# Kernel tuning notes

Hardware: AMD Instinct MI355X
Metric: run time of the kernel (lower is better)

The kernel has to match this reference:

```python
import jax, jax.numpy as jnp
import numpy as np

HEADS = 4
DIM_HEAD = 32
DIM = 128
HIDDEN = HEADS * DIM_HEAD  # 128
LN_EPS = 1e-6


def setup_inputs() -> dict:
    key = jax.random.key(0)
    ks = jax.random.split(key, 4)
    b, X, Y, Z = 4, 32, 32, 32
    x = jax.random.normal(ks[0], (b, X, Y, Z, DIM), dtype=jnp.float32)
    # 1x1x1 convs are pointwise linears: kernel [in, out]
    w_qkv = jax.random.normal(ks[1], (DIM, 3 * HIDDEN), dtype=jnp.float32) * (DIM ** -0.5)
    w_out = jax.random.normal(ks[2], (HIDDEN, DIM), dtype=jnp.float32) * (HIDDEN ** -0.5)
    b_out = jax.random.normal(ks[3], (DIM,), dtype=jnp.float32) * 0.02
    ln_scale = jnp.ones((DIM,), dtype=jnp.float32)
    ln_bias = jnp.zeros((DIM,), dtype=jnp.float32)
    return {"x": x, "w_qkv": w_qkv, "w_out": w_out, "b_out": b_out,
            "ln_scale": ln_scale, "ln_bias": ln_bias}


def reference(x, w_qkv, w_out, b_out, ln_scale, ln_bias):
    b, X, Y, Z, c = x.shape
    n = X * Y * Z
    scale = DIM_HEAD ** (-0.5)

    # 1x1x1 conv (no bias) == pointwise matmul over channels
    qkv = jnp.einsum('bxyzc,cd->bxyzd', x, w_qkv)  # [b,X,Y,Z,3*hidden]
    q, k, v = jnp.split(qkv, 3, axis=-1)

    # rearrange 'b x y z (h c) -> b h c n'
    def to_bhcn(t):
        return t.reshape(b, n, HEADS, DIM_HEAD).transpose(0, 2, 3, 1)

    q, k, v = to_bhcn(q), to_bhcn(k), to_bhcn(v)

    q = jax.nn.softmax(q, axis=-2) * scale   # softmax over feature dim d
    k = jax.nn.softmax(k, axis=-1)           # softmax over token dim n

    context = jnp.einsum('bhdn,bhcn->bhdc', k, v)   # [b,h,d,c] small d=c=32
    out = jnp.einsum('bhde,bhdn->bhen', context, q) # [b,h,e,n]

    # rearrange 'b h c n -> b x y z (h c)' (cubic volume, matching original)
    out = out.transpose(0, 3, 1, 2).reshape(b, X, Y, Z, HIDDEN)

    # final 1x1x1 conv with bias
    out = jnp.einsum('bxyzh,hc->bxyzc', out, w_out) + b_out

    # LayerNorm over last axis (flax default eps=1e-6, with scale+bias)
    mu = jnp.mean(out, axis=-1, keepdims=True)
    var = jnp.mean(jnp.square(out - mu), axis=-1, keepdims=True)
    out = (out - mu) * jax.lax.rsqrt(var + LN_EPS) * ln_scale + ln_bias
    return out
```

## Files before the change

kernel.cpp:

```cpp
#include <hip/hip_runtime.h>
#include <hip/hip_bf16.h>

typedef _Float16 f16;
typedef _Float16 f16x4 __attribute__((ext_vector_type(4)));
typedef _Float16 f16x8 __attribute__((ext_vector_type(8)));
typedef float f32x4 __attribute__((ext_vector_type(4)));

#define MFMA(a, b, c) __builtin_amdgcn_mfma_f32_16x16x32_f16((a), (b), (c), 0, 0, 0)

#define BB 4
#define NPOS 32768
#define HH 4
#define NBLK 1024
#define NBLK3 4096
#define STATB 2304
#define LDP 136

__device__ __forceinline__ f16x8 ldx8(const float* p) {
  float4 a = *(const float4*)p;
  float4 b = *(const float4*)(p + 4);
  return (f16x8){(f16)a.x, (f16)a.y, (f16)a.z, (f16)a.w,
                 (f16)b.x, (f16)b.y, (f16)b.z, (f16)b.w};
}

__global__ __launch_bounds__(256)
void la_k0_prep(const float* __restrict__ wqkv, f16* __restrict__ wkvF,
                f16* __restrict__ wqF) {
  const int g0 = blockIdx.x * 256 + threadIdx.x;
  for (int i = g0; i < 32768; i += 16384) {
    int j = i & 7, l = (i >> 3) & 63, ks = (i >> 9) & 3, nt = (i >> 11) & 3,
        h = i >> 13;
    int n = 16 * nt + (l & 15);
    int c = 32 * ks + 8 * (l >> 4) + j;
    int col = (n < 32) ? (128 + h * 32 + n) : (256 + h * 32 + (n - 32));
    wkvF[i] = (f16)wqkv[c * 384 + col];
  }
  {
    int i = g0;
    int j = i & 7, l = (i >> 3) & 63, ks = (i >> 9) & 3, a = (i >> 11) & 1,
        h = i >> 12;
    int row = l & 15;
    int n = 8 * (row >> 2) + 4 * a + (row & 3);
    int c = 32 * ks + 8 * (l >> 4) + j;
    wqF[i] = (f16)wqkv[c * 384 + h * 32 + n];
  }
}

__global__ __launch_bounds__(256, 4)
void la_k1_stats(const float* __restrict__ x, const f16* __restrict__ wkvF,
                 const f16* __restrict__ wqF, char* __restrict__ stats,
                 f16* __restrict__ Qhat) {
  const int blk = blockIdx.x, t = threadIdx.x;
  const int w = t >> 6, l = t & 63, lg = l >> 4, ln = l & 15;

  __shared__ __align__(16) f16 EV[64 * LDP];

  const float* xb = x + (size_t)blk * (128 * 128);
  f16x8 xf[2][4];
#pragma unroll
  for (int mi = 0; mi < 2; ++mi)
#pragma unroll
    for (int ks = 0; ks < 4; ++ks)
      xf[mi][ks] = ldx8(xb + (32 * w + 16 * mi + ln) * 128 + 32 * ks + 8 * lg);

  const f32x4 Z4 = {0.f, 0.f, 0.f, 0.f};

#pragma unroll 1
  for (int h = 0; h < HH; ++h) {
    f32x4 acc[2][4];
#pragma unroll
    for (int mi = 0; mi < 2; ++mi)
#pragma unroll
      for (int nt = 0; nt < 4; ++nt) acc[mi][nt] = Z4;
#pragma unroll
    for (int ks = 0; ks < 4; ++ks) {
#pragma unroll
      for (int nt = 0; nt < 4; ++nt) {
        f16x8 bf = *(const f16x8*)(wkvF + (((h * 4 + nt) * 4 + ks) << 9) + l * 8);
        acc[0][nt] = MFMA(xf[0][ks], bf, acc[0][nt]);
        acc[1][nt] = MFMA(xf[1][ks], bf, acc[1][nt]);
      }
    }

    {
      float sl[2] = {0.f, 0.f};
#pragma unroll
      for (int nt = 0; nt < 2; ++nt)
#pragma unroll
        for (int mi = 0; mi < 2; ++mi) {
          float e0 = __expf(acc[mi][nt][0]);
          float e1 = __expf(acc[mi][nt][1]);
          float e2 = __expf(acc[mi][nt][2]);
          float e3 = __expf(acc[mi][nt][3]);
          sl[nt] += (e0 + e1) + (e2 + e3);
          *(f16x4*)&EV[(16 * nt + ln) * LDP + 32 * w + 16 * mi + 4 * lg] =
              (f16x4){(f16)e0, (f16)e1, (f16)e2, (f16)e3};
          f32x4 vv = acc[mi][nt + 2];
          *(f16x4*)&EV[(32 + 16 * nt + ln) * LDP + 32 * w + 16 * mi + 4 * lg] =
              (f16x4){(f16)vv[0], (f16)vv[1], (f16)vv[2], (f16)vv[3]};
        }
#pragma unroll
      for (int nt = 0; nt < 2; ++nt) {
        sl[nt] += __shfl_xor(sl[nt], 16);
        sl[nt] += __shfl_xor(sl[nt], 32);
      }
      f16* sp = (f16*)(stats + (size_t)(blk * HH + h) * STATB + 2048);
      if (lg == 0) {
        sp[ln * 4 + w] = (f16)sl[0];
        sp[(16 + ln) * 4 + w] = (f16)sl[1];
      }
    }

    __syncthreads();

    {
      const int tm = w >> 1, tn = w & 1;
      f32x4 tacc = Z4;
#pragma unroll
      for (int ks = 0; ks < 4; ++ks) {
        f16x8 ea = *(const f16x8*)&EV[(16 * tm + ln) * LDP + 32 * ks + 8 * lg];
        f16x8 vb = *(const f16x8*)&EV[(32 + 16 * tn + ln) * LDP + 32 * ks + 8 * lg];
        tacc = MFMA(ea, vb, tacc);
      }
      f16* tp = (f16*)(stats + (size_t)(blk * HH + h) * STATB);
#pragma unroll
      for (int r = 0; r < 4; ++r)
        tp[(16 * tm + 4 * lg + r) * 32 + 16 * tn + ln] = (f16)tacc[r];
    }

    {
      f32x4 qa[2][2];
#pragma unroll
      for (int mi = 0; mi < 2; ++mi)
#pragma unroll
        for (int a = 0; a < 2; ++a) qa[mi][a] = Z4;
#pragma unroll
      for (int ks = 0; ks < 4; ++ks) {
        f16x8 a0 = *(const f16x8*)(wqF + (((h * 2 + 0) * 4 + ks) << 9) + l * 8);
        f16x8 a1 = *(const f16x8*)(wqF + (((h * 2 + 1) * 4 + ks) << 9) + l * 8);
#pragma unroll
        for (int mi = 0; mi < 2; ++mi) {
          qa[mi][0] = MFMA(a0, xf[mi][ks], qa[mi][0]);
          qa[mi][1] = MFMA(a1, xf[mi][ks], qa[mi][1]);
        }
      }
#pragma unroll
      for (int mi = 0; mi < 2; ++mi) {
        float s = 0.f;
#pragma unroll
        for (int a = 0; a < 2; ++a)
#pragma unroll
          for (int r = 0; r < 4; ++r) {
            qa[mi][a][r] = __expf(qa[mi][a][r]);
            s += qa[mi][a][r];
          }
        s += __shfl_xor(s, 16);
        s += __shfl_xor(s, 32);
        const float inv = 0.17677669529663688f / s;
        f16x8 af = (f16x8){(f16)(qa[mi][0][0] * inv), (f16)(qa[mi][0][1] * inv),
                           (f16)(qa[mi][0][2] * inv), (f16)(qa[mi][0][3] * inv),
                           (f16)(qa[mi][1][0] * inv), (f16)(qa[mi][1][1] * inv),
                           (f16)(qa[mi][1][2] * inv), (f16)(qa[mi][1][3] * inv)};
        f16* qp = Qhat + (((size_t)(blk * 8 + 2 * w + mi) * 4 + h) << 9) + l * 8;
        *(f16x8*)qp = af;
      }
    }

    __syncthreads();
  }
}

__global__ __launch_bounds__(256)
void la_k2_combine(const char* __restrict__ stats, f16* __restrict__ ctxN) {
  const int gid = blockIdx.x;
  const int bh = gid >> 5, d = gid & 31;
  const int b = bh >> 2, h = bh & 3;
  const int t = threadIdx.x, w = t >> 6, l = t & 63;
  const int c = t & 31, grp = t >> 5;
  __shared__ float redt[4][32];
  __shared__ float reds[4];

  float sg = 0.f, tc = 0.f;
  for (int i = grp; i < 256; i += 8) {
    const char* ub = stats + (size_t)((b * 256 + i) * HH + h) * STATB;
    tc += (float)((const f16*)ub)[d * 32 + c];
    f16x4 s4 = *(const f16x4*)(ub + 2048 + d * 8);
    sg += ((float)s4[0] + (float)s4[1]) + ((float)s4[2] + (float)s4[3]);
  }
  tc += __shfl_xor(tc, 32);
  sg += __shfl_xor(sg, 32);
  if (l < 32) redt[w][l] = tc;
  if (l == 0) reds[w] = sg;
  __syncthreads();
  if (t < 32) {
    float tt = (redt[0][t] + redt[1][t]) + (redt[2][t] + redt[3][t]);
    float ss = (reds[0] + reds[1]) + (reds[2] + reds[3]);
    ctxN[((size_t)bh * 32 + d) * 32 + t] = (f16)(tt / ss);
  }
}

__global__ __launch_bounds__(256)
void la_k2b_fold(const f16* __restrict__ ctxN, const float* __restrict__ wout,
                 f16* __restrict__ GTF) {
  const int b = blockIdx.x, t = threadIdx.x;
  const int h = t >> 6, l = t & 63, lg = l >> 4, ln = l & 15;
  const f32x4 Z4 = {0.f, 0.f, 0.f, 0.f};

  const f16* cb = ctxN + (size_t)((b * HH + h) * 32) * 32;
  f16x8 bfrag[2];
#pragma unroll
  for (int nt = 0; nt < 2; ++nt)
    bfrag[nt] = *(const f16x8*)(cb + (16 * nt + ln) * 32 + 8 * lg);

  f16* gf = GTF + (size_t)b * 16384;
#pragma unroll
  for (int mt = 0; mt < 8; ++mt) {
    f16x8 af;
#pragma unroll
    for (int j = 0; j < 8; ++j)
      af[j] = (f16)wout[(32 * h + 8 * lg + j) * 128 + 16 * mt + ln];
#pragma unroll
    for (int nt = 0; nt < 2; ++nt) {
      f32x4 acc = MFMA(af, bfrag[nt], Z4);
#pragma unroll
      for (int r = 0; r < 4; ++r) {
        int dsub = 16 * nt + ln;
        gf[((h * 8 + mt) << 9) + (16 * (dsub >> 3) + 4 * lg + r) * 8 + (dsub & 7)] =
            (f16)acc[r];
      }
    }
  }
}

__global__ __launch_bounds__(64)
void la_k3_out(const f16* __restrict__ Qhat, const f16* __restrict__ GTF,
               const float* __restrict__ bout, const float* __restrict__ lns,
               const float* __restrict__ lnb, float* __restrict__ out) {
  const int blk = blockIdx.x;
  const int l = threadIdx.x, lg = l >> 4, ln = l & 15;
  const int b = blk >> 10;

  const f32x4 Z4 = {0.f, 0.f, 0.f, 0.f};
  const f16* gf = GTF + (size_t)b * 16384;

  f16x8 af[2][4];
#pragma unroll
  for (int g = 0; g < 2; ++g)
#pragma unroll
    for (int h = 0; h < HH; ++h)
      af[g][h] = *(const f16x8*)(Qhat +
          (((size_t)(blk * 2 + g) * 4 + h) << 9) + l * 8);

  f32x4 y[2][8];
#pragma unroll
  for (int g = 0; g < 2; ++g)
#pragma unroll
    for (int nc = 0; nc < 8; ++nc) y[g][nc] = Z4;

#pragma unroll
  for (int h = 0; h < HH; ++h) {
#pragma unroll
    for (int nc = 0; nc < 8; ++nc) {
      f16x8 gfr = *(const f16x8*)(gf + (((h * 8 + nc) << 9) + l * 8));
      y[0][nc] = MFMA(gfr, af[0][h], y[0][nc]);
      y[1][nc] = MFMA(gfr, af[1][h], y[1][nc]);
    }
  }

#pragma unroll
  for (int nc = 0; nc < 8; ++nc) {
    f32x4 bb = *(const f32x4*)(bout + 16 * nc + 4 * lg);
    y[0][nc] += bb;
    y[1][nc] += bb;
  }

#pragma unroll
  for (int g = 0; g < 2; ++g) {
    float s = 0.f;
#pragma unroll
    for (int nc = 0; nc < 8; ++nc)
      s += (y[g][nc][0] + y[g][nc][1]) + (y[g][nc][2] + y[g][nc][3]);
    s += __shfl_xor(s, 16);
    s += __shfl_xor(s, 32);
    const float mean = s * (1.f / 128.f);
    float v = 0.f;
#pragma unroll
    for (int nc = 0; nc < 8; ++nc)
#pragma unroll
      for (int r = 0; r < 4; ++r) {
        float dv = y[g][nc][r] - mean;
        v = fmaf(dv, dv, v);
      }
    v += __shfl_xor(v, 16);
    v += __shfl_xor(v, 32);
    const float inv = rsqrtf(v * (1.f / 128.f) + 1e-6f);

    float* op = out + (size_t)(blk * 32 + 16 * g + ln) * 128;
#pragma unroll
    for (int nc = 0; nc < 8; ++nc) {
      f32x4 sv = *(const f32x4*)(lns + 16 * nc + 4 * lg);
      f32x4 b2 = *(const f32x4*)(lnb + 16 * nc + 4 * lg);
      f32x4 o4;
#pragma unroll
      for (int r = 0; r < 4; ++r)
        o4[r] = (y[g][nc][r] - mean) * inv * sv[r] + b2[r];
      *(f32x4*)(op + 16 * nc + 4 * lg) = o4;
    }
  }
}

extern "C" void kernel_launch(void* const* d_in, const int* in_sizes, int n_in,
                              void* d_out, int out_size, void* d_ws, size_t ws_size,
                              hipStream_t stream) {
  const float* x = (const float*)d_in[0];
  const float* w_qkv = (const float*)d_in[1];
  const float* w_out = (const float*)d_in[2];
  const float* b_out = (const float*)d_in[3];
  const float* ln_s = (const float*)d_in[4];
  const float* ln_b = (const float*)d_in[5];
  float* out = (float*)d_out;

  char* ws = (char*)d_ws;
  char* stats = ws;
  f16* wkvF = (f16*)(ws + 9437184);
  f16* wqF = (f16*)(ws + 9437184 + 65536);
  f16* GTF = (f16*)(ws + 9437184 + 65536 + 32768);
  f16* ctxN = (f16*)(ws + 9437184 + 65536 + 32768 + 131072);
  f16* Qhat = (f16*)(ws + 9437184 + 65536 + 32768 + 131072 + 32768);

  la_k0_prep<<<dim3(64), 256, 0, stream>>>(w_qkv, wkvF, wqF);
  la_k1_stats<<<dim3(NBLK), 256, 0, stream>>>(x, wkvF, wqF, stats, Qhat);
  la_k2_combine<<<dim3(512), 256, 0, stream>>>(stats, ctxN);
  la_k2b_fold<<<dim3(BB), 256, 0, stream>>>(ctxN, w_out, GTF);
  la_k3_out<<<dim3(NBLK3), 64, 0, stream>>>(Qhat, GTF, b_out, ln_s, ln_b, out);
}
```

Before: 77.74 us.

## Double stats-kernel block size so each wave handles 16 rows

The stats kernel now runs with 512 threads (8 waves) per block instead of 256, and each wave handles 16 positions instead of 32. Per-wave register use for the x fragments and accumulators is halved, and per-wave partial sums are stored as 8 entries per row, so the stats stride grows and the combine kernel reads 8 partials. The goal is more latency hiding and less register pressure. In exchange, weight fragments are reloaded by twice as many waves, half the waves sit idle during the context MFMA, and the larger block may hit the 4-blocks-per-CU occupancy limit.

```diff
diff --git a/kernel.cpp b/kernel.cpp
--- a/kernel.cpp
+++ b/kernel.cpp
@@ -13,7 +13,7 @@
 #define HH 4
 #define NBLK 1024
 #define NBLK3 4096
-#define STATB 2304
+#define STATB 2560
 #define LDP 136
 
 __device__ __forceinline__ f16x8 ldx8(const float* p) {
@@ -46,7 +46,7 @@
   }
 }
 
-__global__ __launch_bounds__(256, 4)
+__global__ __launch_bounds__(512, 4)
 void la_k1_stats(const float* __restrict__ x, const f16* __restrict__ wkvF,
                  const f16* __restrict__ wqF, char* __restrict__ stats,
                  f16* __restrict__ Qhat) {
@@ -56,49 +56,42 @@
   __shared__ __align__(16) f16 EV[64 * LDP];
 
   const float* xb = x + (size_t)blk * (128 * 128);
-  f16x8 xf[2][4];
-#pragma unroll
-  for (int mi = 0; mi < 2; ++mi)
-#pragma unroll
-    for (int ks = 0; ks < 4; ++ks)
-      xf[mi][ks] = ldx8(xb + (32 * w + 16 * mi + ln) * 128 + 32 * ks + 8 * lg);
+  f16x8 xf[4];
+#pragma unroll
+  for (int ks = 0; ks < 4; ++ks)
+    xf[ks] = ldx8(xb + (16 * w + ln) * 128 + 32 * ks + 8 * lg);
 
   const f32x4 Z4 = {0.f, 0.f, 0.f, 0.f};
 
 #pragma unroll 1
   for (int h = 0; h < HH; ++h) {
-    f32x4 acc[2][4];
-#pragma unroll
-    for (int mi = 0; mi < 2; ++mi)
-#pragma unroll
-      for (int nt = 0; nt < 4; ++nt) acc[mi][nt] = Z4;
+    f32x4 acc[4];
+#pragma unroll
+    for (int nt = 0; nt < 4; ++nt) acc[nt] = Z4;
 #pragma unroll
     for (int ks = 0; ks < 4; ++ks) {
 #pragma unroll
       for (int nt = 0; nt < 4; ++nt) {
         f16x8 bf = *(const f16x8*)(wkvF + (((h * 4 + nt) * 4 + ks) << 9) + l * 8);
-        acc[0][nt] = MFMA(xf[0][ks], bf, acc[0][nt]);
-        acc[1][nt] = MFMA(xf[1][ks], bf, acc[1][nt]);
+        acc[nt] = MFMA(xf[ks], bf, acc[nt]);
       }
     }
 
     {
       float sl[2] = {0.f, 0.f};
 #pragma unroll
-      for (int nt = 0; nt < 2; ++nt)
-#pragma unroll
-        for (int mi = 0; mi < 2; ++mi) {
-          float e0 = __expf(acc[mi][nt][0]);
-          float e1 = __expf(acc[mi][nt][1]);
-          float e2 = __expf(acc[mi][nt][2]);
-          float e3 = __expf(acc[mi][nt][3]);
-          sl[nt] += (e0 + e1) + (e2 + e3);
-          *(f16x4*)&EV[(16 * nt + ln) * LDP + 32 * w + 16 * mi + 4 * lg] =
-              (f16x4){(f16)e0, (f16)e1, (f16)e2, (f16)e3};
-          f32x4 vv = acc[mi][nt + 2];
-          *(f16x4*)&EV[(32 + 16 * nt + ln) * LDP + 32 * w + 16 * mi + 4 * lg] =
-              (f16x4){(f16)vv[0], (f16)vv[1], (f16)vv[2], (f16)vv[3]};
-        }
+      for (int nt = 0; nt < 2; ++nt) {
+        float e0 = __expf(acc[nt][0]);
+        float e1 = __expf(acc[nt][1]);
+        float e2 = __expf(acc[nt][2]);
+        float e3 = __expf(acc[nt][3]);
+        sl[nt] += (e0 + e1) + (e2 + e3);
+        *(f16x4*)&EV[(16 * nt + ln) * LDP + 16 * w + 4 * lg] =
+            (f16x4){(f16)e0, (f16)e1, (f16)e2, (f16)e3};
+        f32x4 vv = acc[nt + 2];
+        *(f16x4*)&EV[(32 + 16 * nt + ln) * LDP + 16 * w + 4 * lg] =
+            (f16x4){(f16)vv[0], (f16)vv[1], (f16)vv[2], (f16)vv[3]};
+      }
 #pragma unroll
       for (int nt = 0; nt < 2; ++nt) {
         sl[nt] += __shfl_xor(sl[nt], 16);
@@ -106,14 +99,14 @@
       }
       f16* sp = (f16*)(stats + (size_t)(blk * HH + h) * STATB + 2048);
       if (lg == 0) {
-        sp[ln * 4 + w] = (f16)sl[0];
-        sp[(16 + ln) * 4 + w] = (f16)sl[1];
+        sp[ln * 8 + w] = (f16)sl[0];
+        sp[(16 + ln) * 8 + w] = (f16)sl[1];
       }
     }
 
     __syncthreads();
 
-    {
+    if (w < 4) {
       const int tm = w >> 1, tn = w & 1;
       f32x4 tacc = Z4;
 #pragma unroll
@@ -129,41 +122,33 @@
     }
 
     {
-      f32x4 qa[2][2];
-#pragma unroll
-      for (int mi = 0; mi < 2; ++mi)
-#pragma unroll
-        for (int a = 0; a < 2; ++a) qa[mi][a] = Z4;
+      f32x4 qa[2];
+      qa[0] = Z4;
+      qa[1] = Z4;
 #pragma unroll
       for (int ks = 0; ks < 4; ++ks) {
         f16x8 a0 = *(const f16x8*)(wqF + (((h * 2 + 0) * 4 + ks) << 9) + l * 8);
         f16x8 a1 = *(const f16x8*)(wqF + (((h * 2 + 1) * 4 + ks) << 9) + l * 8);
-#pragma unroll
-        for (int mi = 0; mi < 2; ++mi) {
-          qa[mi][0] = MFMA(a0, xf[mi][ks], qa[mi][0]);
-          qa[mi][1] = MFMA(a1, xf[mi][ks], qa[mi][1]);
+        qa[0] = MFMA(a0, xf[ks], qa[0]);
+        qa[1] = MFMA(a1, xf[ks], qa[1]);
+      }
+      float s = 0.f;
+#pragma unroll
+      for (int a = 0; a < 2; ++a)
+#pragma unroll
+        for (int r = 0; r < 4; ++r) {
+          qa[a][r] = __expf(qa[a][r]);
+          s += qa[a][r];
         }
-      }
-#pragma unroll
-      for (int mi = 0; mi < 2; ++mi) {
-        float s = 0.f;
-#pragma unroll
-        for (int a = 0; a < 2; ++a)
-#pragma unroll
-          for (int r = 0; r < 4; ++r) {
-            qa[mi][a][r] = __expf(qa[mi][a][r]);
-            s += qa[mi][a][r];
-          }
-        s += __shfl_xor(s, 16);
-        s += __shfl_xor(s, 32);
-        const float inv = 0.17677669529663688f / s;
-        f16x8 af = (f16x8){(f16)(qa[mi][0][0] * inv), (f16)(qa[mi][0][1] * inv),
-                           (f16)(qa[mi][0][2] * inv), (f16)(qa[mi][0][3] * inv),
-                           (f16)(qa[mi][1][0] * inv), (f16)(qa[mi][1][1] * inv),
-                           (f16)(qa[mi][1][2] * inv), (f16)(qa[mi][1][3] * inv)};
-        f16* qp = Qhat + (((size_t)(blk * 8 + 2 * w + mi) * 4 + h) << 9) + l * 8;
-        *(f16x8*)qp = af;
-      }
+      s += __shfl_xor(s, 16);
+      s += __shfl_xor(s, 32);
+      const float inv = 0.17677669529663688f / s;
+      f16x8 af = (f16x8){(f16)(qa[0][0] * inv), (f16)(qa[0][1] * inv),
+                         (f16)(qa[0][2] * inv), (f16)(qa[0][3] * inv),
+                         (f16)(qa[1][0] * inv), (f16)(qa[1][1] * inv),
+                         (f16)(qa[1][2] * inv), (f16)(qa[1][3] * inv)};
+      f16* qp = Qhat + (((size_t)(blk * 8 + w) * 4 + h) << 9) + l * 8;
+      *(f16x8*)qp = af;
     }
 
     __syncthreads();
@@ -184,8 +169,9 @@
   for (int i = grp; i < 256; i += 8) {
     const char* ub = stats + (size_t)((b * 256 + i) * HH + h) * STATB;
     tc += (float)((const f16*)ub)[d * 32 + c];
-    f16x4 s4 = *(const f16x4*)(ub + 2048 + d * 8);
-    sg += ((float)s4[0] + (float)s4[1]) + ((float)s4[2] + (float)s4[3]);
+    f16x8 s8 = *(const f16x8*)(ub + 2048 + d * 16);
+    sg += (((float)s8[0] + (float)s8[1]) + ((float)s8[2] + (float)s8[3])) +
+          (((float)s8[4] + (float)s8[5]) + ((float)s8[6] + (float)s8[7]));
   }
   tc += __shfl_xor(tc, 32);
   sg += __shfl_xor(sg, 32);
@@ -322,14 +308,14 @@
 
   char* ws = (char*)d_ws;
   char* stats = ws;
-  f16* wkvF = (f16*)(ws + 9437184);
-  f16* wqF = (f16*)(ws + 9437184 + 65536);
-  f16* GTF = (f16*)(ws + 9437184 + 65536 + 32768);
-  f16* ctxN = (f16*)(ws + 9437184 + 65536 + 32768 + 131072);
-  f16* Qhat = (f16*)(ws + 9437184 + 65536 + 32768 + 131072 + 32768);
+  f16* wkvF = (f16*)(ws + 10485760);
+  f16* wqF = (f16*)(ws + 10485760 + 65536);
+  f16* GTF = (f16*)(ws + 10485760 + 65536 + 32768);
+  f16* ctxN = (f16*)(ws + 10485760 + 65536 + 32768 + 131072);
+  f16* Qhat = (f16*)(ws + 10485760 + 65536 + 32768 + 131072 + 32768);
 
   la_k0_prep<<<dim3(64), 256, 0, stream>>>(w_qkv, wkvF, wqF);
-  la_k1_stats<<<dim3(NBLK), 256, 0, stream>>>(x, wkvF, wqF, stats, Qhat);
+  la_k1_stats<<<dim3(NBLK), 512, 0, stream>>>(x, wkvF, wqF, stats, Qhat);
   la_k2_combine<<<dim3(512), 256, 0, stream>>>(stats, ctxN);
   la_k2b_fold<<<dim3(BB), 256, 0, stream>>>(ctxN, w_out, GTF);
   la_k3_out<<<dim3(NBLK3), 64, 0, stream>>>(Qhat, GTF, b_out, ln_s, ln_b, out);
```

After: 87.75 us. 1.13x slower.
